# Kernel tuning notes

Hardware: AMD Instinct MI355X
Metric: run time of the kernel (lower is better)

## Reference

```python
import jax, jax.numpy as jnp
import numpy as np

B, N, C = 4, 4096, 128  # batch, tokens (flattened 3D volume), channels
F = 128  # filters


def setup_inputs() -> dict:
    key = jax.random.key(0)
    ks = jax.random.split(key, 7)
    s = 1.0 / np.sqrt(C)
    return {
        "inputs": jax.random.normal(ks[0], (B, N, C), dtype=jnp.float32),
        "Wq": jax.random.normal(ks[1], (C, F), dtype=jnp.float32) * s,
        "bq": jnp.zeros((F,), dtype=jnp.float32),
        "Wk": jax.random.normal(ks[2], (C, F), dtype=jnp.float32) * s,
        "bk": jnp.zeros((F,), dtype=jnp.float32),
        "Wv": jax.random.normal(ks[3], (C, F), dtype=jnp.float32) * s,
        "bv": jnp.zeros((F,), dtype=jnp.float32),
    }


def reference(inputs, Wq, bq, Wk, bk, Wv, bv):
    # Dense projections
    q = inputs @ Wq + bq  # [B, N, F]
    k = inputs @ Wk + bk
    v = inputs @ Wv + bv
    scale = jnp.sqrt(jnp.asarray(F, dtype=q.dtype))
    scores = jnp.einsum("bnf,bmf->bnm", q, k) / scale  # [B, N, N]
    weights = jax.nn.softmax(scores, axis=-1)
    return jnp.einsum("bnm,bmf->bnf", weights, v)
```

## Files before the change

kernel.cpp:

```cpp
#include <hip/hip_runtime.h>

typedef unsigned short u16;
typedef unsigned int u32;
typedef float f32x4 __attribute__((ext_vector_type(4)));
typedef short s16x8 __attribute__((ext_vector_type(8)));
typedef unsigned int u32x2 __attribute__((ext_vector_type(2)));
typedef unsigned int u32x4 __attribute__((ext_vector_type(4)));

#define NB 4
#define NT 4096
#define ND 128
#define NQ (NB * NT)

#define QK_SCALE 0.12751879523138906f

using as3_void = __attribute__((address_space(3))) void;
using as1_void = __attribute__((address_space(1))) void;

__device__ __forceinline__ u16 f2bf(float x){
  unsigned u = __float_as_uint(x);
  return (u16)((u + 0x7FFFu + ((u >> 16) & 1u)) >> 16);
}
__device__ __forceinline__ u32 cvtpk(float lo, float hi){
  u32 r; asm("v_cvt_pk_bf16_f32 %0, %1, %2" : "=v"(r) : "v"(lo), "v"(hi)); return r;
}
__device__ __forceinline__ f32x4 mfma16(s16x8 a, s16x8 b, f32x4 c){
  return __builtin_amdgcn_mfma_f32_16x16x32_bf16(a, b, c, 0, 0, 0);
}

__global__ void k_wprep(const float* __restrict__ Wq, const float* __restrict__ Wk,
                        const float* __restrict__ Wv, u16* __restrict__ WT){
  int mat = blockIdx.x >> 7;
  int f   = blockIdx.x & 127;
  const float* W = (mat == 0) ? Wq : (mat == 1) ? Wk : Wv;
  int c = threadIdx.x;
  WT[mat * 16384 + f * 128 + c] = f2bf(W[c * 128 + f]);
}

__global__ __launch_bounds__(256) void k_proj(
    const float* __restrict__ X, const u16* __restrict__ WT,
    const float* __restrict__ bq, const float* __restrict__ bk, const float* __restrict__ bv,
    u16* __restrict__ Qs, u16* __restrict__ Ks, u16* __restrict__ VTs)
{
  const int lane = threadIdx.x & 63;
  const int w    = threadIdx.x >> 6;
  const int lm = lane & 15, lg = lane >> 4;
  const int rowbase = blockIdx.x * 64 + w * 16;

  s16x8 a[4];
  const float* xr = X + (rowbase + lm) * ND;
  #pragma unroll
  for (int kc = 0; kc < 4; ++kc){
    f32x4 x0 = *(const f32x4*)(xr + kc * 32 + lg * 8);
    f32x4 x1 = *(const f32x4*)(xr + kc * 32 + lg * 8 + 4);
    s16x8 t;
    t[0]=(short)f2bf(x0[0]); t[1]=(short)f2bf(x0[1]); t[2]=(short)f2bf(x0[2]); t[3]=(short)f2bf(x0[3]);
    t[4]=(short)f2bf(x1[0]); t[5]=(short)f2bf(x1[1]); t[6]=(short)f2bf(x1[2]); t[7]=(short)f2bf(x1[3]);
    a[kc] = t;
  }

  #pragma unroll
  for (int mat = 0; mat < 3; ++mat){
    const float* bias = (mat==0) ? bq : (mat==1) ? bk : bv;
    float bl[8];
    #pragma unroll
    for (int n = 0; n < 8; ++n) bl[n] = bias[n * 16 + lm];
    f32x4 acc[8];
    #pragma unroll
    for (int n = 0; n < 8; ++n) acc[n] = f32x4{0.f,0.f,0.f,0.f};
    #pragma unroll
    for (int kc = 0; kc < 4; ++kc){
      #pragma unroll
      for (int n = 0; n < 8; ++n){
        s16x8 bf = *(const s16x8*)&WT[mat*16384 + (n*16 + lm)*128 + kc*32 + lg*8];
        acc[n] = mfma16(a[kc], bf, acc[n]);
      }
    }
    #pragma unroll
    for (int n = 0; n < 8; ++n){
      int f = n * 16 + lm;
      #pragma unroll
      for (int i = 0; i < 4; ++i){
        int r = rowbase + lg * 4 + i;
        float val = acc[n][i] + bl[n];
        if (mat == 0){
          Qs[r * ND + f] = f2bf(val * QK_SCALE);
        } else if (mat == 1){
          Ks[r * ND + (f ^ ((r & 7) << 3))] = f2bf(val);
        } else {
          int bb = r >> 12, nt = r & (NT - 1);
          VTs[(bb * ND + f) * NT + (nt ^ ((f & 3) << 3) ^ (((f >> 2) & 1) << 2))] = f2bf(val);
        }
      }
    }
  }
}

__global__ __launch_bounds__(512, 4) void k_attn(
    const u16* __restrict__ Qs, const u16* __restrict__ Ks,
    const u16* __restrict__ VTs, u16* __restrict__ Op, float* __restrict__ lp)
{
  __shared__ __align__(16) u16 lds[32768];
  __shared__ float lbuf[4][32];
  u16* kbuf = lds;
  u16* vbuf = lds + 16384;

  const int lin = blockIdx.x;
  const int logical = (lin & 7) * 64 + (lin >> 3);
  const int qblk = logical & 127;
  const int quarter = logical >> 7;

  const int lane = threadIdx.x & 63;
  const int w  = threadIdx.x >> 6;
  const int qw = w >> 1, g = w & 1;
  const int lm = lane & 15, lg = lane >> 4;
  const int q0 = qblk * 128 + qw * 32;
  const int b  = q0 >> 12;
  const int kv0 = quarter * 1024 + g * 512;

  s16x8 aq[2][4];
  #pragma unroll
  for (int sq = 0; sq < 2; ++sq){
    const u16* qr = Qs + (size_t)(q0 + sq * 16 + lm) * ND;
    #pragma unroll
    for (int kc = 0; kc < 4; ++kc) aq[sq][kc] = *(const s16x8*)(qr + kc * 32 + lg * 8);
  }

  f32x4 o[2][8];
  #pragma unroll
  for (int sq = 0; sq < 2; ++sq)
    #pragma unroll
    for (int n = 0; n < 8; ++n) o[sq][n] = f32x4{0.f,0.f,0.f,0.f};
  float l_[2] = {0.f, 0.f};

  const u16* gk = Ks  + ((size_t)b * NT + kv0 + qw * 8 + (lane >> 4)) * ND + (lane & 15) * 8;
  const u16* gv = VTs + ((size_t)b * ND + qw * 32 + (lane >> 2)) * NT + kv0 + (lane & 3) * 8;

  auto stage = [&](int buf){
    u16* kd = kbuf + (buf * 2 + g) * 4096 + qw * 1024;
    u16* vd = vbuf + (buf * 2 + g) * 4096 + qw * 1024;
    __builtin_amdgcn_global_load_lds((const as1_void*)gk,
                                     (as3_void*)kd, 16, 0, 0);
    __builtin_amdgcn_global_load_lds((const as1_void*)(gk + (size_t)4 * ND),
                                     (as3_void*)(kd + 512), 16, 0, 0);
    __builtin_amdgcn_global_load_lds((const as1_void*)gv,
                                     (as3_void*)vd, 16, 0, 0);
    __builtin_amdgcn_global_load_lds((const as1_void*)(gv + (size_t)16 * NT),
                                     (as3_void*)(vd + 512), 16, 0, 0);
    gk += (size_t)32 * ND;
    gv += 32;
  };

  const int kswz = (lm & 7) << 3;
  const int vswz = ((lm & 3) << 3) ^ (((lm >> 2) & 1) << 2);
  const int vcol0 = (lg * 4) ^ vswz;
  const int vcol1 = (16 + lg * 4) ^ vswz;

  stage(0);
  __syncthreads();
  int par = 0;

  for (int t = 0; t < 16; ++t){
    if (t < 15) stage(par ^ 1);
    const u16* kb = kbuf + (par * 2 + g) * 4096;
    const u16* vb = vbuf + (par * 2 + g) * 4096;

    f32x4 st[2][2];
    #pragma unroll
    for (int sq = 0; sq < 2; ++sq)
      #pragma unroll
      for (int n = 0; n < 2; ++n) st[sq][n] = f32x4{0.f,0.f,0.f,0.f};
    __builtin_amdgcn_s_setprio(1);
    #pragma unroll
    for (int kc = 0; kc < 4; ++kc){
      #pragma unroll
      for (int n = 0; n < 2; ++n){
        s16x8 kf = *(const s16x8*)&kb[(n * 16 + lm) * 128 + ((kc * 32 + lg * 8) ^ kswz)];
        st[0][n] = mfma16(kf, aq[0][kc], st[0][n]);
        st[1][n] = mfma16(kf, aq[1][kc], st[1][n]);
      }
    }
    __builtin_amdgcn_s_setprio(0);

    s16x8 pa[2];
    #pragma unroll
    for (int sq = 0; sq < 2; ++sq){
      float p[8];
      #pragma unroll
      for (int n = 0; n < 2; ++n)
        #pragma unroll
        for (int i = 0; i < 4; ++i){
          p[n * 4 + i] = __builtin_amdgcn_exp2f(st[sq][n][i]);
          l_[sq] += p[n * 4 + i];
        }
      pa[sq] = __builtin_bit_cast(s16x8, u32x4{
          cvtpk(p[0], p[1]), cvtpk(p[2], p[3]),
          cvtpk(p[4], p[5]), cvtpk(p[6], p[7])});
    }

    __builtin_amdgcn_s_setprio(1);
    #pragma unroll
    for (int nf = 0; nf < 8; ++nf){
      const int vr = (nf * 16 + lm) * 32;
      u32x2 v0 = *(const u32x2*)&vb[vr + vcol0];
      u32x2 v1 = *(const u32x2*)&vb[vr + vcol1];
      s16x8 vf = __builtin_bit_cast(s16x8, u32x4{v0[0], v0[1], v1[0], v1[1]});
      o[0][nf] = mfma16(pa[0], vf, o[0][nf]);
      o[1][nf] = mfma16(pa[1], vf, o[1][nf]);
    }
    __builtin_amdgcn_s_setprio(0);

    __syncthreads();
    par ^= 1;
  }

  #pragma unroll
  for (int sq = 0; sq < 2; ++sq){
    float v = l_[sq];
    v += __shfl_xor(v, 16);
    v += __shfl_xor(v, 32);
    l_[sq] = v;
  }

  float* mbF = (float*)lds;
  __syncthreads();
  if (g == 1){
    #pragma unroll
    for (int sq = 0; sq < 2; ++sq){
      #pragma unroll
      for (int i = 0; i < 4; ++i)
        #pragma unroll
        for (int nf = 0; nf < 8; ++nf)
          mbF[qw * 4096 + (sq * 16 + lg * 4 + i) * 128 + nf * 16 + lm] = o[sq][nf][i];
      if (lg == 0) lbuf[qw][sq * 16 + lm] = l_[sq];
    }
  }
  __syncthreads();
  if (g == 0){
    #pragma unroll
    for (int sq = 0; sq < 2; ++sq){
      l_[sq] += lbuf[qw][sq * 16 + lm];
      #pragma unroll
      for (int i = 0; i < 4; ++i){
        const size_t r = (size_t)quarter * NQ + q0 + sq * 16 + lg * 4 + i;
        #pragma unroll
        for (int nf = 0; nf < 8; ++nf)
          Op[r * ND + nf * 16 + lm] = f2bf(
              o[sq][nf][i] + mbF[qw * 4096 + (sq * 16 + lg * 4 + i) * 128 + nf * 16 + lm]);
      }
      if (lg == 0) lp[(size_t)quarter * NQ + q0 + sq * 16 + lm] = l_[sq];
    }
  }
}

__global__ __launch_bounds__(256) void k_merge(const u16* __restrict__ Op,
                                               const float* __restrict__ lp,
                                               float* __restrict__ Out){
  const int gid = blockIdx.x * 256 + threadIdx.x;
  const int q = gid >> 4, c = gid & 15;
  const float inv = 1.f / (lp[q] + lp[NQ + q] + lp[2 * NQ + q] + lp[3 * NQ + q]);
  float acc[8] = {0,0,0,0,0,0,0,0};
  #pragma unroll
  for (int qt = 0; qt < 4; ++qt){
    s16x8 v = *(const s16x8*)(Op + ((size_t)qt * NQ + q) * ND + c * 8);
    #pragma unroll
    for (int j = 0; j < 8; ++j)
      acc[j] += __uint_as_float(((u32)(u16)v[j]) << 16);
  }
  f32x4 r0{acc[0]*inv, acc[1]*inv, acc[2]*inv, acc[3]*inv};
  f32x4 r1{acc[4]*inv, acc[5]*inv, acc[6]*inv, acc[7]*inv};
  *(f32x4*)(Out + (size_t)q * ND + c * 8)     = r0;
  *(f32x4*)(Out + (size_t)q * ND + c * 8 + 4) = r1;
}

extern "C" void kernel_launch(void* const* d_in, const int* in_sizes, int n_in,
                              void* d_out, int out_size, void* d_ws, size_t ws_size,
                              hipStream_t stream) {
  const float* X  = (const float*)d_in[0];
  const float* Wq = (const float*)d_in[1];
  const float* bq = (const float*)d_in[2];
  const float* Wk = (const float*)d_in[3];
  const float* bk = (const float*)d_in[4];
  const float* Wv = (const float*)d_in[5];
  const float* bv = (const float*)d_in[6];
  float* Out = (float*)d_out;

  u16* Qs  = (u16*)d_ws;
  u16* Ks  = Qs  + (size_t)NQ * ND;
  u16* VTs = Ks  + (size_t)NQ * ND;
  u16* WT  = VTs + (size_t)NQ * ND;
  u16* Op  = WT + 3 * 128 * 128;
  float* lp = (float*)(Op + (size_t)4 * NQ * ND);

  hipLaunchKernelGGL(k_wprep, dim3(3 * 128), dim3(128), 0, stream, Wq, Wk, Wv, WT);
  hipLaunchKernelGGL(k_proj,  dim3(NQ / 64), dim3(256), 0, stream,
                     X, WT, bq, bk, bv, Qs, Ks, VTs);
  hipLaunchKernelGGL(k_attn,  dim3(512), dim3(512), 0, stream, Qs, Ks, VTs, Op, lp);
  hipLaunchKernelGGL(k_merge, dim3(NQ * 16 / 256), dim3(256), 0, stream, Op, lp, Out);
}
```

Measured before the change: 80.93 us.

## Software-pipeline QK and PV stages and coalesce V-transpose stores via LDS

The attention loop is restructured so the PV matmul of the previous tile runs before the QK/softmax of the current tile, with staging of the next tile placed between them. The goal is to overlap exp work with MFMA and hide load latency. The projection kernel now transposes V through a shared-memory tile and writes VTs with 16-byte coalesced stores instead of scattered 2-byte stores. The row-sum accumulation is also reassociated as a tree. The cost is an extra barrier per iteration and more live registers.

```diff
diff --git a/kernel.cpp b/kernel.cpp
--- a/kernel.cpp
+++ b/kernel.cpp
@@ -42,6 +42,7 @@
     const float* __restrict__ bq, const float* __restrict__ bk, const float* __restrict__ bv,
     u16* __restrict__ Qs, u16* __restrict__ Ks, u16* __restrict__ VTs)
 {
+  __shared__ u16 vt[128 * 64];
   const int lane = threadIdx.x & 63;
   const int w    = threadIdx.x >> 6;
   const int lm = lane & 15, lg = lane >> 4;
@@ -88,11 +89,22 @@
         } else if (mat == 1){
           Ks[r * ND + (f ^ ((r & 7) << 3))] = f2bf(val);
         } else {
-          int bb = r >> 12, nt = r & (NT - 1);
-          VTs[(bb * ND + f) * NT + (nt ^ ((f & 3) << 3) ^ (((f >> 2) & 1) << 2))] = f2bf(val);
+          int stcol = (w * 16 + lg * 4 + i) ^ ((f & 3) << 3) ^ (((f >> 2) & 1) << 2);
+          vt[f * 64 + (stcol ^ ((f & 7) << 3))] = f2bf(val);
         }
       }
     }
+  }
+
+  __syncthreads();
+  const int b2  = (blockIdx.x * 64) >> 12;
+  const int nt0 = (blockIdx.x * 64) & (NT - 1);
+  #pragma unroll
+  for (int it = 0; it < 4; ++it){
+    int c = it * 256 + threadIdx.x;
+    int f = c >> 3, ch = c & 7;
+    s16x8 v = *(const s16x8*)&vt[f * 64 + ((ch * 8) ^ ((f & 7) << 3))];
+    *(s16x8*)&VTs[((size_t)b2 * ND + f) * NT + nt0 + ch * 8] = v;
   }
 }
 
@@ -139,12 +151,10 @@
   auto stage = [&](int buf){
     u16* kd = kbuf + (buf * 2 + g) * 4096 + qw * 1024;
     u16* vd = vbuf + (buf * 2 + g) * 4096 + qw * 1024;
-    __builtin_amdgcn_global_load_lds((const as1_void*)gk,
-                                     (as3_void*)kd, 16, 0, 0);
+    __builtin_amdgcn_global_load_lds((const as1_void*)gk, (as3_void*)kd, 16, 0, 0);
     __builtin_amdgcn_global_load_lds((const as1_void*)(gk + (size_t)4 * ND),
                                      (as3_void*)(kd + 512), 16, 0, 0);
-    __builtin_amdgcn_global_load_lds((const as1_void*)gv,
-                                     (as3_void*)vd, 16, 0, 0);
+    __builtin_amdgcn_global_load_lds((const as1_void*)gv, (as3_void*)vd, 16, 0, 0);
     __builtin_amdgcn_global_load_lds((const as1_void*)(gv + (size_t)16 * NT),
                                      (as3_void*)(vd + 512), 16, 0, 0);
     gk += (size_t)32 * ND;
@@ -156,15 +166,9 @@
   const int vcol0 = (lg * 4) ^ vswz;
   const int vcol1 = (16 + lg * 4) ^ vswz;
 
-  stage(0);
-  __syncthreads();
-  int par = 0;
-
-  for (int t = 0; t < 16; ++t){
-    if (t < 15) stage(par ^ 1);
-    const u16* kb = kbuf + (par * 2 + g) * 4096;
-    const u16* vb = vbuf + (par * 2 + g) * 4096;
-
+  s16x8 pa_p[2];
+  auto qk_sm = [&](int buf){
+    const u16* kb = kbuf + (buf * 2 + g) * 4096;
     f32x4 st[2][2];
     #pragma unroll
     for (int sq = 0; sq < 2; ++sq)
@@ -181,23 +185,23 @@
       }
     }
     __builtin_amdgcn_s_setprio(0);
-
-    s16x8 pa[2];
     #pragma unroll
     for (int sq = 0; sq < 2; ++sq){
       float p[8];
       #pragma unroll
       for (int n = 0; n < 2; ++n)
         #pragma unroll
-        for (int i = 0; i < 4; ++i){
+        for (int i = 0; i < 4; ++i)
           p[n * 4 + i] = __builtin_amdgcn_exp2f(st[sq][n][i]);
-          l_[sq] += p[n * 4 + i];
-        }
-      pa[sq] = __builtin_bit_cast(s16x8, u32x4{
+      l_[sq] += ((p[0] + p[1]) + (p[2] + p[3])) + ((p[4] + p[5]) + (p[6] + p[7]));
+      pa_p[sq] = __builtin_bit_cast(s16x8, u32x4{
           cvtpk(p[0], p[1]), cvtpk(p[2], p[3]),
           cvtpk(p[4], p[5]), cvtpk(p[6], p[7])});
     }
-
+  };
+
+  auto pv = [&](int buf){
+    const u16* vb = vbuf + (buf * 2 + g) * 4096;
     __builtin_amdgcn_s_setprio(1);
     #pragma unroll
     for (int nf = 0; nf < 8; ++nf){
@@ -205,14 +209,27 @@
       u32x2 v0 = *(const u32x2*)&vb[vr + vcol0];
       u32x2 v1 = *(const u32x2*)&vb[vr + vcol1];
       s16x8 vf = __builtin_bit_cast(s16x8, u32x4{v0[0], v0[1], v1[0], v1[1]});
-      o[0][nf] = mfma16(pa[0], vf, o[0][nf]);
-      o[1][nf] = mfma16(pa[1], vf, o[1][nf]);
+      o[0][nf] = mfma16(pa_p[0], vf, o[0][nf]);
+      o[1][nf] = mfma16(pa_p[1], vf, o[1][nf]);
     }
     __builtin_amdgcn_s_setprio(0);
-
+  };
+
+  stage(0);
+  __syncthreads();
+  stage(1);
+  qk_sm(0);
+  __syncthreads();
+
+  for (int t = 1; t < 16; ++t){
+    const int par = t & 1;
+    pv(par ^ 1);
     __syncthreads();
-    par ^= 1;
-  }
+    if (t < 15) stage(par ^ 1);
+    qk_sm(par);
+    __syncthreads();
+  }
+  pv(1);
 
   #pragma unroll
   for (int sq = 0; sq < 2; ++sq){
```

After: 85.02 us. 5.1% more time.

## Split projection kernel per matrix and stage V transpose through LDS

Applied to the files above, without the earlier changes.

The projection kernel now launches 768 blocks, each computing one of Q, K or V for 64 rows, instead of 256 blocks computing all three. This triples parallelism, and the block index is remapped so neighbouring blocks pick different matrices. For V, the transposed tile is written into swizzled shared memory and then stored to global memory as 16-byte vector writes, replacing scattered 2-byte strided stores. In exchange, each X row is loaded and converted three times instead of once, and the V path adds a block barrier.

```diff
diff --git a/kernel.cpp b/kernel.cpp
--- a/kernel.cpp
+++ b/kernel.cpp
@@ -42,13 +42,17 @@
     const float* __restrict__ bq, const float* __restrict__ bk, const float* __restrict__ bv,
     u16* __restrict__ Qs, u16* __restrict__ Ks, u16* __restrict__ VTs)
 {
+  __shared__ u16 vt[128 * 64];
   const int lane = threadIdx.x & 63;
   const int w    = threadIdx.x >> 6;
   const int lm = lane & 15, lg = lane >> 4;
-  const int rowbase = blockIdx.x * 64 + w * 16;
+  const int L   = (blockIdx.x & 7) * 96 + (blockIdx.x >> 3);
+  const int mat = L % 3;
+  const int rb  = L / 3;
+  const int rowbase = rb * 64 + w * 16;
 
   s16x8 a[4];
-  const float* xr = X + (rowbase + lm) * ND;
+  const float* xr = X + (size_t)(rowbase + lm) * ND;
   #pragma unroll
   for (int kc = 0; kc < 4; ++kc){
     f32x4 x0 = *(const f32x4*)(xr + kc * 32 + lg * 8);
@@ -59,39 +63,61 @@
     a[kc] = t;
   }
 
-  #pragma unroll
-  for (int mat = 0; mat < 3; ++mat){
-    const float* bias = (mat==0) ? bq : (mat==1) ? bk : bv;
-    float bl[8];
-    #pragma unroll
-    for (int n = 0; n < 8; ++n) bl[n] = bias[n * 16 + lm];
-    f32x4 acc[8];
-    #pragma unroll
-    for (int n = 0; n < 8; ++n) acc[n] = f32x4{0.f,0.f,0.f,0.f};
-    #pragma unroll
-    for (int kc = 0; kc < 4; ++kc){
-      #pragma unroll
-      for (int n = 0; n < 8; ++n){
-        s16x8 bf = *(const s16x8*)&WT[mat*16384 + (n*16 + lm)*128 + kc*32 + lg*8];
-        acc[n] = mfma16(a[kc], bf, acc[n]);
-      }
-    }
+  const float* bias = (mat == 0) ? bq : (mat == 1) ? bk : bv;
+  float bl[8];
+  #pragma unroll
+  for (int n = 0; n < 8; ++n) bl[n] = bias[n * 16 + lm];
+  f32x4 acc[8];
+  #pragma unroll
+  for (int n = 0; n < 8; ++n) acc[n] = f32x4{0.f,0.f,0.f,0.f};
+  #pragma unroll
+  for (int kc = 0; kc < 4; ++kc){
+    #pragma unroll
+    for (int n = 0; n < 8; ++n){
+      s16x8 bf = *(const s16x8*)&WT[mat*16384 + (n*16 + lm)*128 + kc*32 + lg*8];
+      acc[n] = mfma16(a[kc], bf, acc[n]);
+    }
+  }
+
+  if (mat == 0){
     #pragma unroll
     for (int n = 0; n < 8; ++n){
       int f = n * 16 + lm;
       #pragma unroll
       for (int i = 0; i < 4; ++i){
         int r = rowbase + lg * 4 + i;
-        float val = acc[n][i] + bl[n];
-        if (mat == 0){
-          Qs[r * ND + f] = f2bf(val * QK_SCALE);
-        } else if (mat == 1){
-          Ks[r * ND + (f ^ ((r & 7) << 3))] = f2bf(val);
-        } else {
-          int bb = r >> 12, nt = r & (NT - 1);
-          VTs[(bb * ND + f) * NT + (nt ^ ((f & 3) << 3) ^ (((f >> 2) & 1) << 2))] = f2bf(val);
-        }
-      }
+        Qs[(size_t)r * ND + f] = f2bf((acc[n][i] + bl[n]) * QK_SCALE);
+      }
+    }
+  } else if (mat == 1){
+    #pragma unroll
+    for (int n = 0; n < 8; ++n){
+      int f = n * 16 + lm;
+      #pragma unroll
+      for (int i = 0; i < 4; ++i){
+        int r = rowbase + lg * 4 + i;
+        Ks[(size_t)r * ND + (f ^ ((r & 7) << 3))] = f2bf(acc[n][i] + bl[n]);
+      }
+    }
+  } else {
+    #pragma unroll
+    for (int n = 0; n < 8; ++n){
+      int f = n * 16 + lm;
+      #pragma unroll
+      for (int i = 0; i < 4; ++i){
+        int stcol = (w * 16 + lg * 4 + i) ^ ((f & 3) << 3) ^ (((f >> 2) & 1) << 2);
+        vt[f * 64 + (stcol ^ ((f & 7) << 3))] = f2bf(acc[n][i] + bl[n]);
+      }
+    }
+    __syncthreads();
+    const int b2  = (rb * 64) >> 12;
+    const int nt0 = (rb * 64) & (NT - 1);
+    #pragma unroll
+    for (int it = 0; it < 4; ++it){
+      int c = it * 256 + threadIdx.x;
+      int f = c >> 3, ch = c & 7;
+      s16x8 v = *(const s16x8*)&vt[f * 64 + ((ch * 8) ^ ((f & 7) << 3))];
+      *(s16x8*)&VTs[((size_t)b2 * ND + f) * NT + nt0 + ch * 8] = v;
     }
   }
 }
@@ -293,7 +319,7 @@
   float* lp = (float*)(Op + (size_t)4 * NQ * ND);
 
   hipLaunchKernelGGL(k_wprep, dim3(3 * 128), dim3(128), 0, stream, Wq, Wk, Wv, WT);
-  hipLaunchKernelGGL(k_proj,  dim3(NQ / 64), dim3(256), 0, stream,
+  hipLaunchKernelGGL(k_proj,  dim3(768), dim3(256), 0, stream,
                      X, WT, bq, bk, bv, Qs, Ks, VTs);
   hipLaunchKernelGGL(k_attn,  dim3(512), dim3(512), 0, stream, Qs, Ks, VTs, Op, lp);
   hipLaunchKernelGGL(k_merge, dim3(NQ * 16 / 256), dim3(256), 0, stream, Op, lp, Out);
```

Result: no change. 81.17 us (+0.3%).
